# Optimization experiments

Hardware: AMD Instinct MI355X
Metric: run time of the kernel (lower is better)

The kernel has to match this reference:

```python
import jax, jax.numpy as jnp
import numpy as np
from jax import lax

STRIDE = 8  # backbone patch-embed stride


def setup_inputs() -> dict:
    key = jax.random.key(0)
    ks = jax.random.split(key, 5)
    B, H, W = 2, 256, 256
    Cr, Cg, Cout = 256, 5, 256
    N = 65536  # memory bank size
    return {
        "image": jax.random.normal(ks[0], (B, 3, H, W), dtype=jnp.float32),
        "geometry_map": jax.random.uniform(ks[1], (B, Cg, H, W), dtype=jnp.float32),
        "backbone_w": jax.random.normal(ks[2], (Cr, 3, STRIDE, STRIDE), dtype=jnp.float32) * 0.05,
        "backbone_b": jnp.zeros((Cr,), dtype=jnp.float32),
        "fusion_w": jax.random.normal(ks[3], (Cout, Cr + Cg), dtype=jnp.float32) * 0.05,
        "fusion_b": jnp.zeros((Cout,), dtype=jnp.float32),
        "memory_bank": jax.random.normal(ks[4], (N, Cout), dtype=jnp.float32),
    }


def reference(image, geometry_map, backbone_w, backbone_b, fusion_w, fusion_b, memory_bank):
    # --- backbone: patch-embed conv + relu -> (B,Cr,H',W') ---
    feat_rgb = lax.conv_general_dilated(
        image, backbone_w, window_strides=(STRIDE, STRIDE), padding="VALID",
        dimension_numbers=("NCHW", "OIHW", "NCHW"))
    feat_rgb = jax.nn.relu(feat_rgb + backbone_b[None, :, None, None])
    B, Cr, H, W = feat_rgb.shape

    # --- bilinear align of geometry map (align_corners=False semantics) ---
    geo = jax.image.resize(geometry_map, (B, geometry_map.shape[1], H, W), method="bilinear")

    # --- fusion 1x1 conv ---
    fused = jnp.concatenate([feat_rgb, geo], axis=1)           # (B, Cr+Cg, H, W)
    fused = jnp.einsum("oc,bchw->bohw", fusion_w, fused) + fusion_b[None, :, None, None]
    C = fused.shape[1]

    # --- NN min-distance to memory bank (cdist + min) ---
    flat = fused.transpose(0, 2, 3, 1).reshape(-1, C)          # (M, C)
    d2 = (jnp.sum(flat * flat, axis=1)[:, None]
          + jnp.sum(memory_bank * memory_bank, axis=1)[None, :]
          - 2.0 * flat @ memory_bank.T)                        # (M, N)
    min_dist = jnp.sqrt(jnp.maximum(jnp.min(d2, axis=1), 0.0))  # sqrt monotone: min before sqrt
    score_plain = min_dist.reshape(B, H, W)

    # --- geometry reweighting (sigmoid mode, alpha=1.0) ---
    density, opacity, anis = geo[:, 3:4], geo[:, 2:3], geo[:, 4:5]
    base = 0.5 * density + 0.25 * (1.0 - opacity) + 0.25 * anis
    w = 1.0 + jax.nn.sigmoid(4.0 * (base - 0.5))               # (B,1,H,W)
    score_geo = score_plain * w[:, 0]
    return score_plain, score_geo
```

## Files before the change

kernel.cpp:

```cpp
#include <hip/hip_runtime.h>
#include <hip/hip_bf16.h>
#include <stdint.h>

typedef __attribute__((ext_vector_type(8))) short bf16x8;
typedef __attribute__((ext_vector_type(4))) float f32x4;

#define B_    2
#define HIN   256
#define WIN   256
#define HOUT  32
#define WOUT  32
#define CG    5
#define CF    261
#define KDIM  256
#define NP    2048
#define NBANK 65536
#define NCHUNKS 32
#define CHUNK  2048
#define SUBR   64
#define NSUB   32

__device__ inline short f2bf(float f) {
  __hip_bfloat16 h = __float2bfloat16(f);
  return *reinterpret_cast<short*>(&h);
}

__global__ __launch_bounds__(256) void k_resize_h(
    const float* __restrict__ geo, float* __restrict__ tmp)
{
  int idx = blockIdx.x * 256 + threadIdx.x;
  int j = idx & 31, row = (idx >> 5) & 255, bc = idx >> 13;
  const float* src = geo + ((size_t)bc * HIN + row) * WIN;
  float acc = 0.f, norm = 0.f;
  #pragma unroll
  for (int t = 0; t < 16; t++) {
    int k = 8 * j - 4 + t;
    float w = 1.f - fabsf((float)t - 7.5f) * 0.125f;
    if (k >= 0 && k < WIN) { acc += w * src[k]; norm += w; }
  }
  tmp[idx] = acc / norm;
}
__global__ __launch_bounds__(256) void k_resize_v(
    const float* __restrict__ tmp, float* __restrict__ geo_rs)
{
  int idx = blockIdx.x * 256 + threadIdx.x;
  if (idx >= B_ * CG * HOUT * WOUT) return;
  int j = idx & 31, i = (idx >> 5) & 31, bc = idx >> 10;
  const float* col = tmp + (size_t)bc * 8192 + j;
  float acc = 0.f, norm = 0.f;
  #pragma unroll
  for (int t = 0; t < 16; t++) {
    int k = 8 * i - 4 + t;
    float w = 1.f - fabsf((float)t - 7.5f) * 0.125f;
    if (k >= 0 && k < HIN) { acc += w * col[(size_t)k * 32]; norm += w; }
  }
  geo_rs[idx] = acc / norm;
}

__global__ __launch_bounds__(256) void k_repack_fw(
    const float* __restrict__ fw, float* __restrict__ fwp)
{
  int idx = blockIdx.x * 256 + threadIdx.x;
  int o = idx / 264, c = idx % 264;
  fwp[idx] = (c < CF) ? fw[(size_t)o * CF + c] : 0.f;
}

__global__ __launch_bounds__(256) void k_convfuse(
    const float* __restrict__ image, const float* __restrict__ geo_rs,
    const float* __restrict__ bw, const float* __restrict__ bb,
    const float* __restrict__ fwp, const float* __restrict__ fb,
    short* __restrict__ flatb, float* __restrict__ qsq, float* __restrict__ wgt)
{
  __shared__ float patch[3 * 8 * 64];
  __shared__ float fused[8][264];
  __shared__ float red[4][8];
  int t = threadIdx.x;
  int blk = blockIdx.x;
  int b = blk >> 7, rem = blk & 127, h = rem >> 2, wq = rem & 3;
  int w0 = wq * 8;

  #pragma unroll
  for (int j = 0; j < 6; j++) {
    int idx = t + j * 256;
    int c = idx >> 9, r = (idx >> 6) & 7, col = idx & 63;
    patch[idx] = image[(((size_t)(b * 3 + c) * HIN) + 8 * h + r) * WIN + 8 * w0 + col];
  }
  if (t < 24) { int i = t / 3, c = 261 + t % 3; fused[i][c] = 0.f; }
  __syncthreads();

  float acc[8];
  #pragma unroll
  for (int i = 0; i < 8; i++) acc[i] = 0.f;
  const float4* wo4 = (const float4*)(bw + (size_t)t * 192);
  for (int cr = 0; cr < 24; cr++) {
    const float* prow = &patch[cr * 64];
    #pragma unroll
    for (int half = 0; half < 2; half++) {
      float4 w = wo4[cr * 2 + half];
      #pragma unroll
      for (int e = 0; e < 4; e++) {
        float wv = (&w.x)[e];
        int cl = half * 4 + e;
        #pragma unroll
        for (int i = 0; i < 8; i++) acc[i] += wv * prow[i * 8 + cl];
      }
    }
  }
  float bias = bb[t];
  #pragma unroll
  for (int i = 0; i < 8; i++) fused[i][t] = fmaxf(acc[i] + bias, 0.f);
  if (t < 40) {
    int i = t / 5, cg = t % 5;
    fused[i][256 + cg] = geo_rs[((size_t)(b * CG + cg) * HOUT + h) * WOUT + w0 + i];
  }
  __syncthreads();

  #pragma unroll
  for (int i = 0; i < 8; i++) acc[i] = 0.f;
  const float4* fwo4 = (const float4*)(fwp + (size_t)t * 264);
  for (int c4 = 0; c4 < 66; c4++) {
    float4 w = fwo4[c4];
    #pragma unroll
    for (int e = 0; e < 4; e++) {
      float wv = (&w.x)[e];
      int c = c4 * 4 + e;
      #pragma unroll
      for (int i = 0; i < 8; i++) acc[i] += wv * fused[i][c];
    }
  }
  float fbias = fb[t];
  #pragma unroll
  for (int i = 0; i < 8; i++) acc[i] += fbias;

  int lane = t & 63, wvid = t >> 6;
  for (int i = 0; i < 8; i++) {
    int p = b * 1024 + h * 32 + w0 + i;
    flatb[(size_t)p * KDIM + t] = f2bf(acc[i]);
    float s = acc[i] * acc[i];
    for (int m = 1; m < 64; m <<= 1) s += __shfl_xor(s, m);
    if (lane == 0) red[wvid][i] = s;
  }
  __syncthreads();
  if (t < 8) {
    float s = red[0][t] + red[1][t] + red[2][t] + red[3][t];
    int p = b * 1024 + h * 32 + w0 + t;
    qsq[p] = s;
    float den = fused[t][256 + 3], opa = fused[t][256 + 2], ani = fused[t][256 + 4];
    float base = 0.5f * den + 0.25f * (1.f - opa) + 0.25f * ani;
    float sg = 1.f / (1.f + expf(-4.f * (base - 0.5f)));
    wgt[p] = 1.f + sg;
  }
}

__global__ __launch_bounds__(256) void k_bankprep(
    const float* __restrict__ mb, short* __restrict__ mbb, float* __restrict__ msq)
{
  int w = threadIdx.x >> 6, lane = threadIdx.x & 63;
  int row = blockIdx.x * 4 + w;
  const float4 v = reinterpret_cast<const float4*>(mb + (size_t)row * 256)[lane];
  short4 o; o.x = f2bf(v.x); o.y = f2bf(v.y); o.z = f2bf(v.z); o.w = f2bf(v.w);
  reinterpret_cast<short4*>(mbb + (size_t)row * 256)[lane] = o;
  float s = v.x * v.x + v.y * v.y + v.z * v.z + v.w * v.w;
  for (int m = 1; m < 64; m <<= 1) s += __shfl_xor(s, m);
  if (lane == 0) msq[row] = s;
}

__global__ __launch_bounds__(256, 2) void k_distmin(
    const short* __restrict__ Aq, const short* __restrict__ Bb,
    const float* __restrict__ qsq, const float* __restrict__ msq,
    float* __restrict__ partial)
{
  __shared__ __align__(16) unsigned char sB[2][32768];
  __shared__ float red[2][128];
  int t = threadIdx.x;
  int lane = t & 63, wid = t >> 6;
  int wr = wid >> 1, wc = wid & 1;
  const int l15 = lane & 15, l4 = lane >> 4;
  int nc = blockIdx.x, mt = blockIdx.y;
  int m0 = mt * 128;
  const size_t nchunk0 = (size_t)nc * CHUNK;
  const unsigned char* Bbyte = (const unsigned char*)Bb;
  const unsigned char* Abyte = (const unsigned char*)Aq;

#define STAGE(dstbase, nbase) do {                                            \
    _Pragma("unroll")                                                         \
    for (int j = 0; j < 8; j++) {                                             \
      int X = j * 4096 + wid * 1024 + lane * 16;                              \
      int r_ = X >> 9, inrow = X & 511;                                       \
      int srow = inrow ^ ((r_ & 7) << 4);                                     \
      const unsigned char* g = Bbyte + ((size_t)(nbase) + r_) * 512 + srow;   \
      __builtin_amdgcn_global_load_lds(                                       \
          (const __attribute__((address_space(1))) unsigned int*)g,           \
          (__attribute__((address_space(3))) unsigned int*)((dstbase) + j * 4096 + wid * 1024), \
          16, 0, 0);                                                          \
    }                                                                         \
  } while (0)

  bf16x8 af[4][8];
  #pragma unroll
  for (int mi = 0; mi < 4; mi++)
    #pragma unroll
    for (int ks = 0; ks < 8; ks++)
      af[mi][ks] = *(const bf16x8*)(Abyte +
          (size_t)(m0 + wr * 64 + mi * 16 + l15) * 512 + ks * 64 + l4 * 16);

  float vmin[4][4];
  #pragma unroll
  for (int mi = 0; mi < 4; mi++)
    #pragma unroll
    for (int r = 0; r < 4; r++) vmin[mi][r] = 3.4e38f;

  STAGE(&sB[0][0], nchunk0);
  __syncthreads();

  int cur = 0;
  for (int s = 0; s < NSUB; s++) {
    if (s + 1 < NSUB) STAGE(&sB[cur ^ 1][0], nchunk0 + (s + 1) * SUBR);
    const size_t nb = nchunk0 + (size_t)s * SUBR;
    float msq0 = msq[nb + wc * 32 + l15];
    float msq1 = msq[nb + wc * 32 + 16 + l15];
    const unsigned char* buf = &sB[cur][0];

    f32x4 acc[4][2];
    #pragma unroll
    for (int mi = 0; mi < 4; mi++) {
      acc[mi][0] = (f32x4){0.f, 0.f, 0.f, 0.f};
      acc[mi][1] = (f32x4){0.f, 0.f, 0.f, 0.f};
    }
    #pragma unroll
    for (int ks = 0; ks < 8; ks++) {
      bf16x8 b0, b1;
      {
        int n = wc * 32 + l15;
        int off = (n << 9) + ks * 64 + l4 * 16; off ^= (n & 7) << 4;
        b0 = *(const bf16x8*)(buf + off);
      }
      {
        int n = wc * 32 + 16 + l15;
        int off = (n << 9) + ks * 64 + l4 * 16; off ^= (n & 7) << 4;
        b1 = *(const bf16x8*)(buf + off);
      }
      #pragma unroll
      for (int mi = 0; mi < 4; mi++) {
        acc[mi][0] = __builtin_amdgcn_mfma_f32_16x16x32_bf16(af[mi][ks], b0, acc[mi][0], 0, 0, 0);
        acc[mi][1] = __builtin_amdgcn_mfma_f32_16x16x32_bf16(af[mi][ks], b1, acc[mi][1], 0, 0, 0);
      }
    }
    #pragma unroll
    for (int mi = 0; mi < 4; mi++)
      #pragma unroll
      for (int r = 0; r < 4; r++) {
        float v = fminf(msq0 - 2.f * acc[mi][0][r], msq1 - 2.f * acc[mi][1][r]);
        vmin[mi][r] = fminf(vmin[mi][r], v);
      }
    __syncthreads();
    cur ^= 1;
  }
#undef STAGE

  #pragma unroll
  for (int mi = 0; mi < 4; mi++)
    #pragma unroll
    for (int r = 0; r < 4; r++) {
      float v = vmin[mi][r];
      v = fminf(v, __shfl_xor(v, 1));
      v = fminf(v, __shfl_xor(v, 2));
      v = fminf(v, __shfl_xor(v, 4));
      v = fminf(v, __shfl_xor(v, 8));
      if (l15 == 0) red[wc][wr * 64 + mi * 16 + l4 * 4 + r] = v;
    }
  __syncthreads();
  if (t < 128) {
    float v = fminf(red[0][t], red[1][t]);
    float d2 = qsq[m0 + t] + v;
    partial[(size_t)(m0 + t) * NCHUNKS + nc] = fmaxf(d2, 0.f);
  }
}

__global__ __launch_bounds__(256) void k_final(
    const float* __restrict__ partial, const float* __restrict__ wgt,
    float* __restrict__ out)
{
  int q = blockIdx.x * 256 + threadIdx.x;
  const float4* p = (const float4*)(partial + (size_t)q * NCHUNKS);
  float v = 3.4e38f;
  #pragma unroll
  for (int j = 0; j < 8; j++) {
    float4 x = p[j];
    v = fminf(v, fminf(fminf(x.x, x.y), fminf(x.z, x.w)));
  }
  float sp = sqrtf(v);
  out[q] = sp;
  out[NP + q] = sp * wgt[q];
}

extern "C" void kernel_launch(void* const* d_in, const int* in_sizes, int n_in,
                              void* d_out, int out_size, void* d_ws, size_t ws_size,
                              hipStream_t stream) {
  const float* image    = (const float*)d_in[0];
  const float* geometry = (const float*)d_in[1];
  const float* bw       = (const float*)d_in[2];
  const float* bb       = (const float*)d_in[3];
  const float* fw       = (const float*)d_in[4];
  const float* fb       = (const float*)d_in[5];
  const float* mb       = (const float*)d_in[6];
  float* out = (float*)d_out;
  char* ws = (char*)d_ws;

  float* geo_rs  = (float*)(ws);
  float* tmp_rs  = (float*)(ws + 40960);
  float* wgt     = (float*)(ws + 368640);
  float* qsq     = (float*)(ws + 376832);
  float* msq     = (float*)(ws + 385024);
  float* fwp     = (float*)(ws + 647168);
  short* flatb   = (short*)(ws + 917504);
  float* partial = (float*)(ws + 1966080);
  short* mbb     = (short*)(ws + 2228224);

  hipLaunchKernelGGL(k_resize_h,  dim3(320),      dim3(256), 0, stream, geometry, tmp_rs);
  hipLaunchKernelGGL(k_resize_v,  dim3(40),       dim3(256), 0, stream, tmp_rs, geo_rs);
  hipLaunchKernelGGL(k_repack_fw, dim3(264),      dim3(256), 0, stream, fw, fwp);
  hipLaunchKernelGGL(k_convfuse,  dim3(256),      dim3(256), 0, stream, image, geo_rs, bw, bb, fwp, fb, flatb, qsq, wgt);
  hipLaunchKernelGGL(k_bankprep,  dim3(16384),    dim3(256), 0, stream, mb, mbb, msq);
  hipLaunchKernelGGL(k_distmin,   dim3(32, 16),   dim3(256), 0, stream, flatb, mbb, qsq, msq, partial);
  hipLaunchKernelGGL(k_final,     dim3(8),        dim3(256), 0, stream, partial, wgt, out);
}
```

Measured before the change: 217.8 us.

## Fuse prep kernels and restructure distmin pipeline with explicit waitcnt barriers

```diff
diff --git a/kernel.cpp b/kernel.cpp
--- a/kernel.cpp
+++ b/kernel.cpp
@@ -5,56 +5,17 @@
 typedef __attribute__((ext_vector_type(8))) short bf16x8;
 typedef __attribute__((ext_vector_type(4))) float f32x4;
 
-#define B_    2
-#define HIN   256
-#define WIN   256
-#define HOUT  32
-#define WOUT  32
-#define CG    5
-#define CF    261
-#define KDIM  256
-#define NP    2048
+#define NP 2048
 #define NBANK 65536
 #define NCHUNKS 32
-#define CHUNK  2048
-#define SUBR   64
-#define NSUB   32
+#define CHUNK 2048
+#define SUBR 64
+#define NSUB 32
+#define CF 261
 
 __device__ inline short f2bf(float f) {
   __hip_bfloat16 h = __float2bfloat16(f);
   return *reinterpret_cast<short*>(&h);
-}
-
-__global__ __launch_bounds__(256) void k_resize_h(
-    const float* __restrict__ geo, float* __restrict__ tmp)
-{
-  int idx = blockIdx.x * 256 + threadIdx.x;
-  int j = idx & 31, row = (idx >> 5) & 255, bc = idx >> 13;
-  const float* src = geo + ((size_t)bc * HIN + row) * WIN;
-  float acc = 0.f, norm = 0.f;
-  #pragma unroll
-  for (int t = 0; t < 16; t++) {
-    int k = 8 * j - 4 + t;
-    float w = 1.f - fabsf((float)t - 7.5f) * 0.125f;
-    if (k >= 0 && k < WIN) { acc += w * src[k]; norm += w; }
-  }
-  tmp[idx] = acc / norm;
-}
-__global__ __launch_bounds__(256) void k_resize_v(
-    const float* __restrict__ tmp, float* __restrict__ geo_rs)
-{
-  int idx = blockIdx.x * 256 + threadIdx.x;
-  if (idx >= B_ * CG * HOUT * WOUT) return;
-  int j = idx & 31, i = (idx >> 5) & 31, bc = idx >> 10;
-  const float* col = tmp + (size_t)bc * 8192 + j;
-  float acc = 0.f, norm = 0.f;
-  #pragma unroll
-  for (int t = 0; t < 16; t++) {
-    int k = 8 * i - 4 + t;
-    float w = 1.f - fabsf((float)t - 7.5f) * 0.125f;
-    if (k >= 0 && k < HIN) { acc += w * col[(size_t)k * 32]; norm += w; }
-  }
-  geo_rs[idx] = acc / norm;
 }
 
 __global__ __launch_bounds__(256) void k_repack_fw(
@@ -65,104 +26,137 @@
   fwp[idx] = (c < CF) ? fw[(size_t)o * CF + c] : 0.f;
 }
 
-__global__ __launch_bounds__(256) void k_convfuse(
-    const float* __restrict__ image, const float* __restrict__ geo_rs,
+__global__ __launch_bounds__(512) void k_prep(
+    const float* __restrict__ image, const float* __restrict__ geometry,
     const float* __restrict__ bw, const float* __restrict__ bb,
     const float* __restrict__ fwp, const float* __restrict__ fb,
-    short* __restrict__ flatb, float* __restrict__ qsq, float* __restrict__ wgt)
+    const float* __restrict__ mb,
+    short* __restrict__ flatb, float* __restrict__ qsq, float* __restrict__ wgt,
+    short* __restrict__ mbb, float* __restrict__ msq)
 {
-  __shared__ float patch[3 * 8 * 64];
-  __shared__ float fused[8][264];
-  __shared__ float red[4][8];
+  __shared__ float patch[1536];
+  __shared__ float fusedS[8][264];
+  __shared__ float gv[40][8];
+  __shared__ float gw[40][8];
+  __shared__ float redS[8][8];
   int t = threadIdx.x;
-  int blk = blockIdx.x;
-  int b = blk >> 7, rem = blk & 127, h = rem >> 2, wq = rem & 3;
-  int w0 = wq * 8;
-
-  #pragma unroll
-  for (int j = 0; j < 6; j++) {
-    int idx = t + j * 256;
+  int bid = blockIdx.x;
+
+  if (bid >= 256) {
+    int row = (bid - 256) * 8 + (t >> 6);
+    int lane = t & 63;
+    float4 v = ((const float4*)(mb + (size_t)row * 256))[lane];
+    short4 o; o.x = f2bf(v.x); o.y = f2bf(v.y); o.z = f2bf(v.z); o.w = f2bf(v.w);
+    ((short4*)(mbb + (size_t)row * 256))[lane] = o;
+    float s = v.x*v.x + v.y*v.y + v.z*v.z + v.w*v.w;
+    #pragma unroll
+    for (int m = 1; m < 64; m <<= 1) s += __shfl_xor(s, m);
+    if (lane == 0) msq[row] = s;
+    return;
+  }
+
+  int b = bid >> 7, rem = bid & 127, h = rem >> 2, w0 = (rem & 3) * 8;
+
+  #pragma unroll
+  for (int j = 0; j < 3; j++) {
+    int idx = t + j * 512;
     int c = idx >> 9, r = (idx >> 6) & 7, col = idx & 63;
-    patch[idx] = image[(((size_t)(b * 3 + c) * HIN) + 8 * h + r) * WIN + 8 * w0 + col];
-  }
-  if (t < 24) { int i = t / 3, c = 261 + t % 3; fused[i][c] = 0.f; }
-  __syncthreads();
-
-  float acc[8];
-  #pragma unroll
-  for (int i = 0; i < 8; i++) acc[i] = 0.f;
-  const float4* wo4 = (const float4*)(bw + (size_t)t * 192);
+    patch[idx] = image[(((size_t)(b*3 + c) * 256) + 8*h + r) * 256 + 8*w0 + col];
+  }
+  if (t >= 320 && t < 344) {
+    int i = (t - 320) / 3, c = 261 + (t - 320) % 3;
+    fusedS[i][c] = 0.f;
+  }
+  if (t < 320) {
+    int v = t >> 3, sub = t & 7;
+    int i = v / 5, cg = v % 5;
+    int jj = w0 + i;
+    float val = 0.f, ws = 0.f;
+    const float* gch = geometry + (size_t)(b*5 + cg) * 65536;
+    #pragma unroll
+    for (int rr = 0; rr < 2; rr++) {
+      int r = sub * 2 + rr;
+      int gr = 8*h - 4 + r;
+      float wr = 1.f - fabsf((float)r - 7.5f) * 0.125f;
+      if (gr >= 0 && gr < 256) {
+        const float* grow = gch + (size_t)gr * 256;
+        for (int c = 0; c < 16; c++) {
+          int gc = 8*jj - 4 + c;
+          if (gc >= 0 && gc < 256) {
+            float wc_ = 1.f - fabsf((float)c - 7.5f) * 0.125f;
+            val += wr * wc_ * grow[gc];
+            ws  += wr * wc_;
+          }
+        }
+      }
+    }
+    gv[v][sub] = val; gw[v][sub] = ws;
+  }
+  __syncthreads();
+  if (t < 40) {
+    int i = t / 5, cg = t % 5;
+    float sv = 0.f, sw = 0.f;
+    #pragma unroll
+    for (int u = 0; u < 8; u++) { sv += gv[t][u]; sw += gw[t][u]; }
+    fusedS[i][256 + cg] = sv / sw;
+  }
+
+  int g = t >> 8, o = t & 255;
+  float a4[4] = {0.f, 0.f, 0.f, 0.f};
+  const float4* wo4 = (const float4*)(bw + (size_t)o * 192);
   for (int cr = 0; cr < 24; cr++) {
-    const float* prow = &patch[cr * 64];
+    const float* prow = &patch[cr * 64 + g * 32];
     #pragma unroll
     for (int half = 0; half < 2; half++) {
-      float4 w = wo4[cr * 2 + half];
+      float4 w4 = wo4[cr*2 + half];
       #pragma unroll
       for (int e = 0; e < 4; e++) {
-        float wv = (&w.x)[e];
-        int cl = half * 4 + e;
+        float wv = (&w4.x)[e];
+        int cl = half*4 + e;
         #pragma unroll
-        for (int i = 0; i < 8; i++) acc[i] += wv * prow[i * 8 + cl];
+        for (int i4 = 0; i4 < 4; i4++) a4[i4] += wv * prow[i4*8 + cl];
       }
     }
   }
-  float bias = bb[t];
-  #pragma unroll
-  for (int i = 0; i < 8; i++) fused[i][t] = fmaxf(acc[i] + bias, 0.f);
-  if (t < 40) {
-    int i = t / 5, cg = t % 5;
-    fused[i][256 + cg] = geo_rs[((size_t)(b * CG + cg) * HOUT + h) * WOUT + w0 + i];
-  }
-  __syncthreads();
-
-  #pragma unroll
-  for (int i = 0; i < 8; i++) acc[i] = 0.f;
-  const float4* fwo4 = (const float4*)(fwp + (size_t)t * 264);
+  float bias = bb[o];
+  #pragma unroll
+  for (int i4 = 0; i4 < 4; i4++) fusedS[g*4 + i4][o] = fmaxf(a4[i4] + bias, 0.f);
+  __syncthreads();
+
+  #pragma unroll
+  for (int i4 = 0; i4 < 4; i4++) a4[i4] = 0.f;
+  const float4* fwo4 = (const float4*)(fwp + (size_t)o * 264);
   for (int c4 = 0; c4 < 66; c4++) {
-    float4 w = fwo4[c4];
+    float4 w4 = fwo4[c4];
     #pragma unroll
     for (int e = 0; e < 4; e++) {
-      float wv = (&w.x)[e];
-      int c = c4 * 4 + e;
+      float wv = (&w4.x)[e];
+      int c = c4*4 + e;
       #pragma unroll
-      for (int i = 0; i < 8; i++) acc[i] += wv * fused[i][c];
-    }
-  }
-  float fbias = fb[t];
-  #pragma unroll
-  for (int i = 0; i < 8; i++) acc[i] += fbias;
-
-  int lane = t & 63, wvid = t >> 6;
-  for (int i = 0; i < 8; i++) {
-    int p = b * 1024 + h * 32 + w0 + i;
-    flatb[(size_t)p * KDIM + t] = f2bf(acc[i]);
-    float s = acc[i] * acc[i];
+      for (int i4 = 0; i4 < 4; i4++) a4[i4] += wv * fusedS[g*4 + i4][c];
+    }
+  }
+  float fbias = fb[o];
+  int lane = t & 63, wid = t >> 6;
+  #pragma unroll
+  for (int i4 = 0; i4 < 4; i4++) {
+    a4[i4] += fbias;
+    int p = b*1024 + h*32 + w0 + g*4 + i4;
+    flatb[(size_t)p * 256 + o] = f2bf(a4[i4]);
+    float s = a4[i4] * a4[i4];
+    #pragma unroll
     for (int m = 1; m < 64; m <<= 1) s += __shfl_xor(s, m);
-    if (lane == 0) red[wvid][i] = s;
+    if (lane == 0) redS[g*4 + i4][wid & 3] = s;
   }
   __syncthreads();
   if (t < 8) {
-    float s = red[0][t] + red[1][t] + red[2][t] + red[3][t];
-    int p = b * 1024 + h * 32 + w0 + t;
+    float s = redS[t][0] + redS[t][1] + redS[t][2] + redS[t][3];
+    int p = b*1024 + h*32 + w0 + t;
     qsq[p] = s;
-    float den = fused[t][256 + 3], opa = fused[t][256 + 2], ani = fused[t][256 + 4];
-    float base = 0.5f * den + 0.25f * (1.f - opa) + 0.25f * ani;
-    float sg = 1.f / (1.f + expf(-4.f * (base - 0.5f)));
-    wgt[p] = 1.f + sg;
-  }
-}
-
-__global__ __launch_bounds__(256) void k_bankprep(
-    const float* __restrict__ mb, short* __restrict__ mbb, float* __restrict__ msq)
-{
-  int w = threadIdx.x >> 6, lane = threadIdx.x & 63;
-  int row = blockIdx.x * 4 + w;
-  const float4 v = reinterpret_cast<const float4*>(mb + (size_t)row * 256)[lane];
-  short4 o; o.x = f2bf(v.x); o.y = f2bf(v.y); o.z = f2bf(v.z); o.w = f2bf(v.w);
-  reinterpret_cast<short4*>(mbb + (size_t)row * 256)[lane] = o;
-  float s = v.x * v.x + v.y * v.y + v.z * v.z + v.w * v.w;
-  for (int m = 1; m < 64; m <<= 1) s += __shfl_xor(s, m);
-  if (lane == 0) msq[row] = s;
+    float den = fusedS[t][256+3], opa = fusedS[t][256+2], ani = fusedS[t][256+4];
+    float base2 = 0.5f*den + 0.25f*(1.f - opa) + 0.25f*ani;
+    wgt[p] = 1.f + 1.f/(1.f + expf(-4.f*(base2 - 0.5f)));
+  }
 }
 
 __global__ __launch_bounds__(256, 2) void k_distmin(
@@ -171,6 +165,7 @@
     float* __restrict__ partial)
 {
   __shared__ __align__(16) unsigned char sB[2][32768];
+  __shared__ float msq_lds[2048];
   __shared__ float red[2][128];
   int t = threadIdx.x;
   int lane = t & 63, wid = t >> 6;
@@ -179,84 +174,116 @@
   int nc = blockIdx.x, mt = blockIdx.y;
   int m0 = mt * 128;
   const size_t nchunk0 = (size_t)nc * CHUNK;
-  const unsigned char* Bbyte = (const unsigned char*)Bb;
+  const unsigned char* Bbyte = (const unsigned char*)Bb + nchunk0 * 512;
   const unsigned char* Abyte = (const unsigned char*)Aq;
 
-#define STAGE(dstbase, nbase) do {                                            \
+  int soff[8];
+  #pragma unroll
+  for (int j = 0; j < 8; j++) {
+    int sh = j * 4 + wid;
+    int ks = sh & 7, hh = (sh >> 3) & 1, wcs = sh >> 4;
+    int n = wcs * 32 + hh * 16 + l15;
+    int k = ks * 64 + l4 * 16;
+    soff[j] = n * 512 + k;
+  }
+
+  {
+    const float4* src = (const float4*)(msq + nchunk0);
+    float4* dst = (float4*)msq_lds;
+    dst[t] = src[t];
+    dst[t + 256] = src[t + 256];
+  }
+
+  bf16x8 af[4][8];
+  #pragma unroll
+  for (int mi = 0; mi < 4; mi++)
+    #pragma unroll
+    for (int ks = 0; ks < 8; ks++) {
+      af[mi][ks] = *(const bf16x8*)(Abyte +
+          (size_t)(m0 + wr*64 + mi*16 + l15) * 512 + ks*64 + l4*16);
+      asm volatile("" : "+v"(af[mi][ks]));
+    }
+
+  float vmin[4][4];
+  #pragma unroll
+  for (int mi = 0; mi < 4; mi++)
+    #pragma unroll
+    for (int r = 0; r < 4; r++) vmin[mi][r] = 3.4e38f;
+
+  __syncthreads();
+
+#define STAGE(bufsel, sidx) do {                                              \
+    const unsigned char* gb_ = Bbyte + (size_t)(sidx) * 32768;                \
+    unsigned char* lb_ = &sB[bufsel][0] + wid * 1024;                         \
     _Pragma("unroll")                                                         \
-    for (int j = 0; j < 8; j++) {                                             \
-      int X = j * 4096 + wid * 1024 + lane * 16;                              \
-      int r_ = X >> 9, inrow = X & 511;                                       \
-      int srow = inrow ^ ((r_ & 7) << 4);                                     \
-      const unsigned char* g = Bbyte + ((size_t)(nbase) + r_) * 512 + srow;   \
+    for (int j_ = 0; j_ < 8; j_++) {                                          \
       __builtin_amdgcn_global_load_lds(                                       \
-          (const __attribute__((address_space(1))) unsigned int*)g,           \
-          (__attribute__((address_space(3))) unsigned int*)((dstbase) + j * 4096 + wid * 1024), \
-          16, 0, 0);                                                          \
+        (const __attribute__((address_space(1))) unsigned int*)(gb_ + soff[j_]), \
+        (__attribute__((address_space(3))) unsigned int*)(lb_ + j_*4096),     \
+        16, 0, 0);                                                            \
     }                                                                         \
   } while (0)
 
-  bf16x8 af[4][8];
-  #pragma unroll
-  for (int mi = 0; mi < 4; mi++)
-    #pragma unroll
-    for (int ks = 0; ks < 8; ks++)
-      af[mi][ks] = *(const bf16x8*)(Abyte +
-          (size_t)(m0 + wr * 64 + mi * 16 + l15) * 512 + ks * 64 + l4 * 16);
-
-  float vmin[4][4];
-  #pragma unroll
-  for (int mi = 0; mi < 4; mi++)
-    #pragma unroll
-    for (int r = 0; r < 4; r++) vmin[mi][r] = 3.4e38f;
-
-  STAGE(&sB[0][0], nchunk0);
-  __syncthreads();
-
-  int cur = 0;
-  for (int s = 0; s < NSUB; s++) {
-    if (s + 1 < NSUB) STAGE(&sB[cur ^ 1][0], nchunk0 + (s + 1) * SUBR);
-    const size_t nb = nchunk0 + (size_t)s * SUBR;
-    float msq0 = msq[nb + wc * 32 + l15];
-    float msq1 = msq[nb + wc * 32 + 16 + l15];
-    const unsigned char* buf = &sB[cur][0];
-
-    f32x4 acc[4][2];
-    #pragma unroll
-    for (int mi = 0; mi < 4; mi++) {
-      acc[mi][0] = (f32x4){0.f, 0.f, 0.f, 0.f};
-      acc[mi][1] = (f32x4){0.f, 0.f, 0.f, 0.f};
-    }
-    #pragma unroll
-    for (int ks = 0; ks < 8; ks++) {
-      bf16x8 b0, b1;
-      {
-        int n = wc * 32 + l15;
-        int off = (n << 9) + ks * 64 + l4 * 16; off ^= (n & 7) << 4;
-        b0 = *(const bf16x8*)(buf + off);
-      }
-      {
-        int n = wc * 32 + 16 + l15;
-        int off = (n << 9) + ks * 64 + l4 * 16; off ^= (n & 7) << 4;
-        b1 = *(const bf16x8*)(buf + off);
-      }
-      #pragma unroll
-      for (int mi = 0; mi < 4; mi++) {
-        acc[mi][0] = __builtin_amdgcn_mfma_f32_16x16x32_bf16(af[mi][ks], b0, acc[mi][0], 0, 0, 0);
-        acc[mi][1] = __builtin_amdgcn_mfma_f32_16x16x32_bf16(af[mi][ks], b1, acc[mi][1], 0, 0, 0);
-      }
-    }
-    #pragma unroll
-    for (int mi = 0; mi < 4; mi++)
-      #pragma unroll
-      for (int r = 0; r < 4; r++) {
-        float v = fminf(msq0 - 2.f * acc[mi][0][r], msq1 - 2.f * acc[mi][1][r]);
-        vmin[mi][r] = fminf(vmin[mi][r], v);
-      }
-    __syncthreads();
-    cur ^= 1;
-  }
+#define ACQUIRE(N) do {                                                       \
+    asm volatile("s_waitcnt vmcnt(" #N ")" ::: "memory");                     \
+    __builtin_amdgcn_s_barrier();                                             \
+    __builtin_amdgcn_sched_barrier(0);                                        \
+  } while (0)
+
+#define RELEASE() do {                                                        \
+    asm volatile("s_waitcnt lgkmcnt(0)" ::: "memory");                        \
+    __builtin_amdgcn_s_barrier();                                             \
+    __builtin_amdgcn_sched_barrier(0);                                        \
+  } while (0)
+
+#define COMPUTE(sarg) do {                                                    \
+    const unsigned char* buf_ = &sB[(sarg) & 1][0] + wc * 16384;              \
+    float m0_ = msq_lds[(sarg) * 64 + wc * 32 + l15];                         \
+    float m1_ = msq_lds[(sarg) * 64 + wc * 32 + 16 + l15];                    \
+    f32x4 acc_[4][2];                                                         \
+    _Pragma("unroll")                                                         \
+    for (int mi = 0; mi < 4; mi++) {                                          \
+      acc_[mi][0] = (f32x4){0.f,0.f,0.f,0.f};                                 \
+      acc_[mi][1] = (f32x4){0.f,0.f,0.f,0.f};                                 \
+    }                                                                         \
+    __builtin_amdgcn_s_setprio(1);                                            \
+    _Pragma("unroll")                                                         \
+    for (int ks = 0; ks < 8; ks++) {                                          \
+      bf16x8 b0_ = *(const bf16x8*)(buf_ + ks*1024 + l4*256 + l15*16);        \
+      bf16x8 b1_ = *(const bf16x8*)(buf_ + 8192 + ks*1024 + l4*256 + l15*16); \
+      _Pragma("unroll")                                                       \
+      for (int mi = 0; mi < 4; mi++) {                                        \
+        acc_[mi][0] = __builtin_amdgcn_mfma_f32_16x16x32_bf16(af[mi][ks], b0_, acc_[mi][0], 0, 0, 0); \
+        acc_[mi][1] = __builtin_amdgcn_mfma_f32_16x16x32_bf16(af[mi][ks], b1_, acc_[mi][1], 0, 0, 0); \
+      }                                                                       \
+    }                                                                         \
+    __builtin_amdgcn_s_setprio(0);                                            \
+    _Pragma("unroll")                                                         \
+    for (int mi = 0; mi < 4; mi++)                                            \
+      _Pragma("unroll")                                                       \
+      for (int r = 0; r < 4; r++)                                             \
+        vmin[mi][r] = fminf(vmin[mi][r],                                      \
+            fminf(m0_ - 2.f*acc_[mi][0][r], m1_ - 2.f*acc_[mi][1][r]));       \
+  } while (0)
+
+  STAGE(0, 0);
+  STAGE(1, 1);
+
+  for (int s = 0; s < NSUB - 2; s++) {
+    ACQUIRE(8);
+    COMPUTE(s);
+    RELEASE();
+    STAGE(s & 1, s + 2);
+  }
+  ACQUIRE(8);
+  COMPUTE(NSUB - 2);
+  ACQUIRE(0);
+  COMPUTE(NSUB - 1);
+
 #undef STAGE
+#undef ACQUIRE
+#undef RELEASE
+#undef COMPUTE
 
   #pragma unroll
   for (int mi = 0; mi < 4; mi++)
@@ -307,21 +334,17 @@
   float* out = (float*)d_out;
   char* ws = (char*)d_ws;
 
-  float* geo_rs  = (float*)(ws);
-  float* tmp_rs  = (float*)(ws + 40960);
-  float* wgt     = (float*)(ws + 368640);
-  float* qsq     = (float*)(ws + 376832);
-  float* msq     = (float*)(ws + 385024);
-  float* fwp     = (float*)(ws + 647168);
-  short* flatb   = (short*)(ws + 917504);
-  float* partial = (float*)(ws + 1966080);
-  short* mbb     = (short*)(ws + 2228224);
-
-  hipLaunchKernelGGL(k_resize_h,  dim3(320),      dim3(256), 0, stream, geometry, tmp_rs);
-  hipLaunchKernelGGL(k_resize_v,  dim3(40),       dim3(256), 0, stream, tmp_rs, geo_rs);
-  hipLaunchKernelGGL(k_repack_fw, dim3(264),      dim3(256), 0, stream, fw, fwp);
-  hipLaunchKernelGGL(k_convfuse,  dim3(256),      dim3(256), 0, stream, image, geo_rs, bw, bb, fwp, fb, flatb, qsq, wgt);
-  hipLaunchKernelGGL(k_bankprep,  dim3(16384),    dim3(256), 0, stream, mb, mbb, msq);
-  hipLaunchKernelGGL(k_distmin,   dim3(32, 16),   dim3(256), 0, stream, flatb, mbb, qsq, msq, partial);
-  hipLaunchKernelGGL(k_final,     dim3(8),        dim3(256), 0, stream, partial, wgt, out);
-}
+  float* wgt     = (float*)(ws);
+  float* qsq     = (float*)(ws + 8192);
+  float* msq     = (float*)(ws + 16384);
+  float* fwp     = (float*)(ws + 278528);
+  short* flatb   = (short*)(ws + 548864);
+  float* partial = (float*)(ws + 1597440);
+  short* mbb     = (short*)(ws + 1859584);
+
+  hipLaunchKernelGGL(k_repack_fw, dim3(264),     dim3(256), 0, stream, fw, fwp);
+  hipLaunchKernelGGL(k_prep,      dim3(8448),    dim3(512), 0, stream,
+                     image, geometry, bw, bb, fwp, fb, mb, flatb, qsq, wgt, mbb, msq);
+  hipLaunchKernelGGL(k_distmin,   dim3(32, 16),  dim3(256), 0, stream, flatb, mbb, qsq, msq, partial);
+  hipLaunchKernelGGL(k_final,     dim3(8),       dim3(256), 0, stream, partial, wgt, out);
+}
```

Result: no change. 214.6 us (-1.5%).
